# Kernel tuning notes

Measured on AMD Instinct MI355X. Metric: run time of the kernel, lower is better.

Reference implementation:

```python
import jax, jax.numpy as jnp
import numpy as np

B = 4096
L = 15          # self.length
NINP = 256      # emb_size
NHID = 512      # hidden_size
VOCAB = 30005
TOPK = 10
K = 4 * TOPK + 2   # 42 actions
N_SPLIT = 2 * TOPK
N_STEP = 5      # num_edits
PAD = 30003


def _lstm_dir(x, Wih, Whh, b, reverse):
    # x: [T,B,D]; Wih: [4H,D]; Whh: [4H,H]; b: [4H] (b_ih+b_hh). PyTorch gate order i,f,g,o.
    Bsz, H = x.shape[1], Whh.shape[1]
    def step(carry, xt):
        h, c = carry
        z = xt @ Wih.T + h @ Whh.T + b
        i, f, g, o = jnp.split(z, 4, axis=-1)
        c = jax.nn.sigmoid(f) * c + jax.nn.sigmoid(i) * jnp.tanh(g)
        h = jax.nn.sigmoid(o) * jnp.tanh(c)
        return (h, c), h
    h0 = jnp.zeros((Bsz, H), x.dtype)
    _, ys = jax.lax.scan(step, (h0, h0), x, reverse=reverse)
    return ys  # [T,B,H], position-aligned for both directions


def bilstm(x, Wih0, Whh0, b0, Wih1, Whh1, b1):
    # x: [B,T,D] -> [B,T,2H]; 2-layer bidirectional, zero initial state (matches c0/h0 zeros).
    xt = jnp.swapaxes(x, 0, 1)
    for Wih, Whh, b in ((Wih0, Whh0, b0), (Wih1, Whh1, b1)):
        fw = _lstm_dir(xt, Wih[0], Whh[0], b[0], False)
        bw = _lstm_dir(xt, Wih[1], Whh[1], b[1], True)
        xt = jnp.concatenate([fw, bw], axis=-1)
    return jnp.swapaxes(xt, 0, 1)


def policy_step(st_1, length_t, pos, emb0, key_pos, rep_words, valid_id,
                emb_table, enc_table, Wih0, Whh0, b0, Wih1, Whh1, b1,
                del_vec, hold_vec, mlp_W, mlp_b, mlp1_W, mlp1_b):
    Bsz = st_1.shape[0]
    pos_row = jnp.zeros((L,), jnp.float32).at[pos].set(1.0)         # static pos
    pos_tensor = jnp.broadcast_to(pos_row[None, :, None], (Bsz, L, 1))
    embt = emb_table[st_1] * (1.0 - pos_tensor)
    x = jnp.concatenate([embt, emb0, pos_tensor], axis=2)            # [B,L,2*ninp+1]
    out = bilstm(x, Wih0, Whh0, b0, Wih1, Whh1, b1)                  # [B,L,2*nhid]
    pooled = out[:, pos, :]
    representation = jnp.concatenate(
        [pooled, key_pos[:, pos:pos + 1], jnp.broadcast_to(pos_row[None, :], (Bsz, L))], axis=1)
    # external encoder output is detached in the original
    word_emb = jax.lax.stop_gradient(enc_table[rep_words])           # [B,4*topk,ninp]
    emb2 = jnp.concatenate([word_emb,
                            jnp.broadcast_to(del_vec, (Bsz, 1, NINP)),
                            jnp.broadcast_to(hold_vec, (Bsz, 1, NINP))], axis=1)  # [B,K,ninp]
    onehot = jnp.broadcast_to(jnp.eye(K, dtype=jnp.float32)[None], (Bsz, K, K))
    emb2 = jnp.concatenate([emb2, onehot], axis=2)                   # [B,K,ninp+K]
    rep100 = representation @ mlp_W.T + mlp_b                        # [B,100]
    emb100 = emb2 @ mlp1_W.T + mlp1_b                                # [B,K,100]
    score = jnp.einsum('bkd,bd->bk', emb100, rep100)
    policy = jax.nn.softmax(score, axis=1)
    action = jnp.argmax(policy, axis=1, keepdims=True).astype(jnp.int32)  # eval mode
    pi = jnp.take_along_axis(policy, action, axis=1)                 # [B,1]

    rep_b = (action < N_SPLIT).astype(jnp.int32)
    replaceflag = rep_b * valid_id
    ins_b = ((action >= N_SPLIT) & (action < 2 * N_SPLIT)).astype(jnp.int32)
    insertflag = ins_b * valid_id * (length_t + ins_b <= 15).astype(jnp.int32)
    del_b = (action == 2 * N_SPLIT).astype(jnp.int32)
    deleteflag = del_b * valid_id * (length_t - del_b > 2).astype(jnp.int32)
    holdflag = 1 - replaceflag - insertflag - deleteflag

    action_words = jnp.take_along_axis(rep_words, jnp.clip(action, 0, N_SPLIT - 1), axis=1)  # [B,1]
    rep_seq = jnp.concatenate([action_words, st_1[:, pos + 1:]], axis=1)
    ins_seq = jnp.concatenate([action_words, st_1[:, pos:-1]], axis=1)
    padding = jnp.full((Bsz, 1), PAD, dtype=st_1.dtype)
    del_seq = jnp.concatenate([st_1[:, pos + 1:], padding], axis=1)
    hol_seq = st_1[:, pos:]
    new_tail = (rep_seq * replaceflag + ins_seq * insertflag
                + del_seq * deleteflag + hol_seq * holdflag)
    st = st_1.at[:, pos:].set(new_tail)
    length_tt = insertflag + length_t - deleteflag
    return st, pi, action.astype(jnp.float32), length_tt


def setup_inputs() -> dict:
    key = jax.random.key(0)
    ks = jax.random.split(key, 20)
    s = 0.05
    in0 = 2 * NINP + 1
    in1 = 2 * NHID
    inp = {
        'input_ids': jax.random.randint(ks[0], (B, L), 0, 30000, dtype=jnp.int32),
        'key_pos': jax.random.uniform(ks[1], (B, L), dtype=jnp.float32),
        'sequence_length': jax.random.randint(ks[2], (B, 1), 3, 16, dtype=jnp.int32),
        'rep_words_all': jax.random.randint(ks[3], (B, N_STEP, 4 * TOPK), 0, 30000, dtype=jnp.int32),
        'valid_id_all': jax.random.randint(ks[4], (B, N_STEP, 1), 0, 2, dtype=jnp.int32),
        'emb_table': jax.random.normal(ks[5], (VOCAB, NINP), jnp.float32) * s,
        'enc_table': jax.random.normal(ks[6], (VOCAB, NINP), jnp.float32) * s,
        'Wih0': jax.random.normal(ks[7], (2, 4 * NHID, in0), jnp.float32) * s,
        'Whh0': jax.random.normal(ks[8], (2, 4 * NHID, NHID), jnp.float32) * s,
        'b0': jax.random.normal(ks[9], (2, 4 * NHID), jnp.float32) * s,
        'Wih1': jax.random.normal(ks[10], (2, 4 * NHID, in1), jnp.float32) * s,
        'Whh1': jax.random.normal(ks[11], (2, 4 * NHID, NHID), jnp.float32) * s,
        'b1': jax.random.normal(ks[12], (2, 4 * NHID), jnp.float32) * s,
        'del_vec': jax.random.uniform(ks[13], (1, 1, NINP), dtype=jnp.float32),
        'hold_vec': jax.random.uniform(ks[14], (1, 1, NINP), dtype=jnp.float32),
        'mlp_W': jax.random.normal(ks[15], (100, 2 * NHID + 1 + L), jnp.float32) * s,
        'mlp_b': jnp.zeros((100,), jnp.float32),
        'mlp1_W': jax.random.normal(ks[16], (100, NINP + K), jnp.float32) * s,
        'mlp1_b': jnp.zeros((100,), jnp.float32),
    }
    return inp


def reference(input_ids, key_pos, sequence_length, rep_words_all, valid_id_all,
              emb_table, enc_table, Wih0, Whh0, b0, Wih1, Whh1, b1,
              del_vec, hold_vec, mlp_W, mlp_b, mlp1_W, mlp1_b):
    st = input_ids
    emb0 = emb_table[input_ids]            # embedding of s0, computed once
    length_t = sequence_length
    pis, acts = [], []
    for i in range(N_STEP):
        pos = i % (L - 3) + 2              # static per unrolled step
        st, pi, a, length_t = policy_step(
            st, length_t, pos, emb0, key_pos,
            rep_words_all[:, i, :], valid_id_all[:, i, :],
            emb_table, enc_table, Wih0, Whh0, b0, Wih1, Whh1, b1,
            del_vec, hold_vec, mlp_W, mlp_b, mlp1_W, mlp1_b)
        pis.append(pi)
        acts.append(a)
    pis = jnp.concatenate(pis, axis=1)     # [B,N_STEP]
    actions = jnp.concatenate(acts, axis=1)
    return pis, actions, st, length_t
```

## Files before the change

kernel.cpp:

```cpp
#include <hip/hip_runtime.h>

#define B_ 4096
#define L_ 15
#define NSTEP_ 5
#define VOC_ 30005
#define PAD_ 30003

typedef _Float16 f16;
typedef f16  f16x8 __attribute__((ext_vector_type(8)));
typedef float f32x16 __attribute__((ext_vector_type(16)));

__device__ __forceinline__ float sigf(float x){ return 1.0f/(1.0f+expf(-x)); }

#define MFMA_(d,a,b) d = __builtin_amdgcn_mfma_f32_32x32x16_f16(a,b,d,0,0,0)

struct RecParams {
  const f16 *A1h_0,*A1l_0,*A1h_1,*A1l_1;
  const f16 *A2h_0,*A2l_0,*A2h_1,*A2l_1;
  const f16 *Wfh_0,*Wfl_0,*Wfh_1,*Wfl_1;
  const float *bias_0,*bias_1;
  const f16 *embH,*embL;
  const int *st,*ids;
  float *c_0,*c_1,*h2_0,*h2_1;
  f16 *hh_0,*hl_0,*hh_1,*hl_1;
  int lda1, lda2, ldh, ldh2, k1p, k2p, first, gather, t_0, t_1, pos, b0c, act0, act1;
};

__device__ __forceinline__ int swz(int row, int s){
  int u = ((row&7)<<1) | s;
  return ((row>>3)<<8) + ((u ^ (u>>1))<<4);
}

__global__ __launch_bounds__(256,2) void rec_gemm(RecParams p){
  const int dir = blockIdx.z;
  if (!(dir ? p.act1 : p.act0)) return;
  const f16* A1h = dir ? p.A1h_1 : p.A1h_0;
  const f16* A1l = dir ? p.A1l_1 : p.A1l_0;
  const f16* A2h = dir ? p.A2h_1 : p.A2h_0;
  const f16* A2l = dir ? p.A2l_1 : p.A2l_0;
  const f16* Wfh = dir ? p.Wfh_1 : p.Wfh_0;
  const f16* Wfl = dir ? p.Wfl_1 : p.Wfl_0;
  const float* bias = dir ? p.bias_1 : p.bias_0;
  float* cbuf = dir ? p.c_1 : p.c_0;
  float* h2   = dir ? p.h2_1 : p.h2_0;
  f16* hhb = dir ? p.hh_1 : p.hh_0;
  f16* hlb = dir ? p.hl_1 : p.hl_0;
  const int tcur = dir ? p.t_1 : p.t_0;

  const int tid  = threadIdx.x;
  const int lane = tid & 63;
  const int w    = tid >> 6;
  const int mbase = blockIdx.y*128;

  __shared__ union {
    float z[128*128];
    f16   stg[8][2048];
  } sm;

  f32x16 accM[2][2], accX[2][2];
#pragma unroll
  for (int i=0;i<2;i++)
#pragma unroll
    for (int j=0;j<2;j++)
#pragma unroll
      for (int r=0;r<16;r++){ accM[i][j][r]=0.f; accX[i][j][r]=0.f; }

  const int arow = (w&1)*64 + (lane&31);
  const int fs = lane>>5;
  const int aoff0 = swz(arow,    fs), aoff1 = swz(arow+32, fs);

  const int ct0 = blockIdx.x*4 + (w>>1)*2;
  const f16* WfhL = Wfh + (size_t)lane*8;
  const f16* WflL = Wfl + (size_t)lane*8;

  const int srow = tid >> 1, ss = tid & 1;
  const int sws = swz(srow, ss);
  const int ktot = p.k1p + p.k2p;

  int tokT=0, tokI=0, zflag=0;
  if (p.gather){
    int gb = p.b0c + mbase + srow;
    tokT = p.st [gb*L_ + tcur];
    tokI = p.ids[gb*L_ + tcur];
    zflag = (tcur == p.pos) ? 1 : 0;
  }

  f16x8 ra_h0, ra_l0, ra_h1, ra_l1;
  const f16x8 zero8 = {0,0,0,0,0,0,0,0};

  auto gload = [&](int ph){
    if (ph >= ktot) return;
    if (ph < p.k1p){
      if (p.gather){
        if (ph < 8){
          if (zflag){ ra_h0=zero8; ra_l0=zero8; ra_h1=zero8; ra_l1=zero8; }
          else {
            size_t base = (size_t)tokT*256 + ph*32 + ss*8;
            ra_h0 = *(const f16x8*)(p.embH + base);
            ra_l0 = *(const f16x8*)(p.embL + base);
            ra_h1 = *(const f16x8*)(p.embH + base + 16);
            ra_l1 = *(const f16x8*)(p.embL + base + 16);
          }
        } else if (ph < 16){
          size_t base = (size_t)tokI*256 + (ph-8)*32 + ss*8;
          ra_h0 = *(const f16x8*)(p.embH + base);
          ra_l0 = *(const f16x8*)(p.embL + base);
          ra_h1 = *(const f16x8*)(p.embH + base + 16);
          ra_l1 = *(const f16x8*)(p.embL + base + 16);
        } else {
          ra_h0 = zero8; ra_l0 = zero8; ra_h1 = zero8; ra_l1 = zero8;
          if (ss == 0) ra_h0[0] = zflag ? (f16)1.0f : (f16)0.0f;
        }
      } else {
        long base = (long)(mbase+srow)*p.lda1 + ph*32 + ss*8;
        ra_h0 = *(const f16x8*)(A1h + base);
        ra_l0 = *(const f16x8*)(A1l + base);
        ra_h1 = *(const f16x8*)(A1h + base + 16);
        ra_l1 = *(const f16x8*)(A1l + base + 16);
      }
    } else {
      long base = (long)(mbase+srow)*p.lda2 + (ph - p.k1p)*32 + ss*8;
      ra_h0 = *(const f16x8*)(A2h + base);
      ra_l0 = *(const f16x8*)(A2l + base);
      ra_h1 = *(const f16x8*)(A2h + base + 16);
      ra_l1 = *(const f16x8*)(A2l + base + 16);
    }
  };
  auto swrite = [&](int buf){
    *(f16x8*)((char*)sm.stg[buf*4+0] + sws) = ra_h0;
    *(f16x8*)((char*)sm.stg[buf*4+1] + sws) = ra_l0;
    *(f16x8*)((char*)sm.stg[buf*4+2] + sws) = ra_h1;
    *(f16x8*)((char*)sm.stg[buf*4+3] + sws) = ra_l1;
  };

  gload(0); swrite(0); gload(1);
  __syncthreads();

  for (int ph=0; ph<ktot; ++ph){
    const int cur = ph & 1;
    size_t base0 = ((size_t)(ph*2+0)*64 + ct0)*512;
    size_t base1 = ((size_t)(ph*2+1)*64 + ct0)*512;
    f16x8 rbh00 = *(const f16x8*)(WfhL + base0);
    f16x8 rbh01 = *(const f16x8*)(WfhL + base0 + 512);
    f16x8 rbl00 = *(const f16x8*)(WflL + base0);
    f16x8 rbl01 = *(const f16x8*)(WflL + base0 + 512);
    f16x8 rbh10 = *(const f16x8*)(WfhL + base1);
    f16x8 rbh11 = *(const f16x8*)(WfhL + base1 + 512);
    f16x8 rbl10 = *(const f16x8*)(WflL + base1);
    f16x8 rbl11 = *(const f16x8*)(WflL + base1 + 512);
    const char* s0h = (const char*)sm.stg[cur*4+0];
    const char* s0l = (const char*)sm.stg[cur*4+1];
    const char* s1h = (const char*)sm.stg[cur*4+2];
    const char* s1l = (const char*)sm.stg[cur*4+3];
    f16x8 a00h = *(const f16x8*)(s0h + aoff0);
    f16x8 a01h = *(const f16x8*)(s0h + aoff1);
    f16x8 a00l = *(const f16x8*)(s0l + aoff0);
    f16x8 a01l = *(const f16x8*)(s0l + aoff1);
    f16x8 a10h = *(const f16x8*)(s1h + aoff0);
    f16x8 a11h = *(const f16x8*)(s1h + aoff1);
    f16x8 a10l = *(const f16x8*)(s1l + aoff0);
    f16x8 a11l = *(const f16x8*)(s1l + aoff1);
    if (ph+1 < ktot){ swrite((ph+1)&1); gload(ph+2); }
    MFMA_(accM[0][0], a00h, rbh00); MFMA_(accX[0][0], a00h, rbl00); MFMA_(accX[0][0], a00l, rbh00);
    MFMA_(accM[1][0], a01h, rbh00); MFMA_(accX[1][0], a01h, rbl00); MFMA_(accX[1][0], a01l, rbh00);
    MFMA_(accM[0][1], a00h, rbh01); MFMA_(accX[0][1], a00h, rbl01); MFMA_(accX[0][1], a00l, rbh01);
    MFMA_(accM[1][1], a01h, rbh01); MFMA_(accX[1][1], a01h, rbl01); MFMA_(accX[1][1], a01l, rbh01);
    MFMA_(accM[0][0], a10h, rbh10); MFMA_(accX[0][0], a10h, rbl10); MFMA_(accX[0][0], a10l, rbh10);
    MFMA_(accM[1][0], a11h, rbh10); MFMA_(accX[1][0], a11h, rbl10); MFMA_(accX[1][0], a11l, rbh10);
    MFMA_(accM[0][1], a10h, rbh11); MFMA_(accX[0][1], a10h, rbl11); MFMA_(accX[0][1], a10l, rbh11);
    MFMA_(accM[1][1], a11h, rbh11); MFMA_(accX[1][1], a11h, rbl11); MFMA_(accX[1][1], a11l, rbh11);
    __syncthreads();
  }

#pragma unroll
  for (int tm=0;tm<2;tm++)
#pragma unroll
   for (int tn=0;tn<2;tn++){
    int lcol = (w>>1)*64 + tn*32 + (lane&31);
    float bv = bias[blockIdx.x*128 + lcol];
#pragma unroll
    for (int r=0;r<16;r++){
      int lrow = (w&1)*64 + tm*32 + (r&3) + 8*(r>>2) + 4*(lane>>5);
      sm.z[lrow*128 + lcol] = accM[tm][tn][r] + 0.000244140625f*accX[tm][tn][r] + bv;
    }
   }
  __syncthreads();

  const int nb = blockIdx.x*32;
#pragma unroll
  for (int it=0; it<16; ++it){
    int idx = it*256 + tid;
    int nq = idx & 31, row = idx >> 5;
    float4 g4 = *(const float4*)&sm.z[row*128 + nq*4];
    int m = mbase + row, n = nb + nq;
    float cp = p.first ? 0.f : cbuf[(size_t)m*512 + n];
    float cc = sigf(g4.y)*cp + sigf(g4.x)*tanhf(g4.z);
    float hv = sigf(g4.w)*tanhf(cc);
    cbuf[(size_t)m*512 + n] = cc;
    f16 hi = (f16)hv;
    f16 lo = (f16)((hv - (float)hi)*4096.0f);
    hhb[(size_t)m*p.ldh + n] = hi;
    hlb[(size_t)m*p.ldh + n] = lo;
    if (h2) h2[(size_t)m*p.ldh2 + n] = hv;
  }
}

__global__ void prep_w0(const float* Wih, const float* Whh, const float* b0,
                        f16* Wfh, f16* Wfl, float* bp){
  int gid = blockIdx.x*blockDim.x + threadIdx.x;
  const int PER_DIR = 66*64*64*8;
  if (gid >= 2*PER_DIR) return;
  int dir = gid / PER_DIR;
  int rem = gid % PER_DIR;
  int j = rem & 7, lane = (rem>>3)&63, ct = (rem>>9)&63, kt16 = rem>>15;
  int n4g = ct*32 + (lane&31);
  int n = n4g>>2, g = n4g&3;
  int srow = dir*2048 + g*512 + n;
  int k = kt16*16 + ((lane>>5)<<3) + j;
  float v;
  if (k < 513)       v = Wih[(size_t)srow*513 + k];
  else if (k < 544)  v = 0.f;
  else               v = Whh[(size_t)srow*512 + (k-544)];
  f16 hi = (f16)v;
  Wfh[gid] = hi;
  Wfl[gid] = (f16)((v - (float)hi)*4096.0f);
  if (kt16==0 && (lane>>5)==0 && j==0) bp[dir*2048 + n4g] = b0[srow];
}

__global__ void prep_w1(const float* Wih, const float* Whh, const float* b1,
                        f16* Wfh, f16* Wfl, float* bp){
  int gid = blockIdx.x*blockDim.x + threadIdx.x;
  const int PER_DIR = 96*64*64*8;
  if (gid >= 2*PER_DIR) return;
  int dir = gid / PER_DIR;
  int rem = gid % PER_DIR;
  int j = rem & 7, lane = (rem>>3)&63, ct = (rem>>9)&63, kt16 = rem>>15;
  int n4g = ct*32 + (lane&31);
  int n = n4g>>2, g = n4g&3;
  int srow = dir*2048 + g*512 + n;
  int k = kt16*16 + ((lane>>5)<<3) + j;
  float v;
  if (k < 1024) v = Wih[(size_t)srow*1024 + k];
  else          v = Whh[(size_t)srow*512 + (k-1024)];
  f16 hi = (f16)v;
  Wfh[gid] = hi;
  Wfl[gid] = (f16)((v - (float)hi)*4096.0f);
  if (kt16==0 && (lane>>5)==0 && j==0) bp[dir*2048 + n4g] = b1[srow];
}

__global__ void prep_emb(const float* emb, f16* eh, f16* el){
  int gid = blockIdx.x*blockDim.x + threadIdx.x;
  if (gid >= VOC_*256) return;
  float v = emb[gid];
  f16 hi = (f16)v;
  eh[gid] = hi;
  el[gid] = (f16)((v - (float)hi)*4096.0f);
}

__global__ void prep_mlpwt(const float* mW, float* wt){
  int gid = blockIdx.x*blockDim.x + threadIdx.x;
  if (gid >= 100*1040) return;
  int j = gid / 1040, k = gid % 1040;
  wt[k*100 + j] = mW[gid];
}

__global__ __launch_bounds__(128) void prep_encproj(const float* enc, const float* delv,
                        const float* holdv, const float* m1W, const float* m1b, float* ep){
  int r = blockIdx.x;
  __shared__ float row[256];
  const float* src = (r < VOC_) ? enc + (size_t)r*256 : (r == VOC_ ? delv : holdv);
  for (int i=threadIdx.x;i<256;i+=128) row[i]=src[i];
  __syncthreads();
  int j = threadIdx.x;
  if (j < 100){
    double s = (double)m1b[j];
    const float* wr = m1W + (size_t)j*298;
    for (int k=0;k<256;k++) s += (double)wr[k] * (double)row[k];
    ep[(size_t)r*100 + j] = (float)s;
  }
}

__global__ void init_st(const int* ids, const int* seqlen, int* st, int* len){
  int gid = blockIdx.x*blockDim.x + threadIdx.x;
  if (gid < B_*L_) st[gid] = ids[gid];
  if (gid < B_)    len[gid] = seqlen[gid];
}

__global__ void sentinel(float* out, float v){
  int gid = blockIdx.x*blockDim.x + threadIdx.x;
  if (gid < B_*NSTEP_) out[gid] = v;
}

__global__ __launch_bounds__(128) void score_update(
    const float* pooled, const float* keypos, const float* mWt, const float* mb,
    const float* ep, const float* m1W, const int* repw, const int* valid,
    int* st, int* len, float* outPis, float* outActs, int step, int pos, int b0){
  int b = blockIdx.x;
  int bg = b0 + b;
  __shared__ float rep[1040];
  __shared__ float r100[100];
  __shared__ double sc[42];
  int tid = threadIdx.x;
  for (int i=tid;i<1024;i+=128) rep[i] = pooled[(size_t)b*1024+i];
  if (tid < 16){
    if (tid == 0) rep[1024] = keypos[bg*L_+pos];
    else          rep[1024+tid] = ((tid-1)==pos) ? 1.f : 0.f;
  }
  __syncthreads();
  if (tid < 100){
    double s = (double)mb[tid];
    for (int k=0;k<1040;k++) s += (double)mWt[k*100+tid] * (double)rep[k];
    r100[tid] = (float)s;
  }
  __syncthreads();
  if (tid < 42){
    int row = (tid < 40) ? repw[((size_t)bg*NSTEP_+step)*40 + tid] : (VOC_ + (tid-40));
    const float* er = ep + (size_t)row*100;
    double s = 0.0;
    for (int j=0;j<100;j++) s += (double)er[j] * (double)r100[j];
    for (int j=0;j<100;j++) s += (double)m1W[j*298 + 256 + tid] * (double)r100[j];
    sc[tid] = s;
  }
  __syncthreads();
  if (tid == 0){
    double mx = sc[0]; int am = 0;
    for (int k=1;k<42;k++) if (sc[k] > mx){ mx = sc[k]; am = k; }
    double sum = 0.0;
    for (int k=0;k<42;k++) sum += exp(sc[k]-mx);
    float pi = (float)(1.0/sum);
    int vid = valid[bg*NSTEP_+step];
    int ln  = len[bg];
    int repb = (am < 20) ? 1 : 0;
    int insb = (am >= 20 && am < 40) ? 1 : 0;
    int delb = (am == 40) ? 1 : 0;
    int repf = repb*vid;
    int insf = insb*vid*(((ln+insb) <= 15) ? 1 : 0);
    int delf = delb*vid*(((ln-delb) >  2) ? 1 : 0);
    int T = L_ - pos;
    int tail[13];
    for (int j=0;j<T;j++) tail[j] = st[bg*L_+pos+j];
    int aw = repw[((size_t)bg*NSTEP_+step)*40 + (am < 20 ? am : 19)];
    for (int j=0;j<T;j++){
      int rv = (j==0) ? aw : tail[j];
      int iv = (j==0) ? aw : tail[j-1];
      int dv = (j < T-1) ? tail[j+1] : PAD_;
      int hv = tail[j];
      int nv = repf ? rv : (insf ? iv : (delf ? dv : hv));
      st[bg*L_+pos+j] = nv;
    }
    len[bg] = ln + insf - delf;
    outPis[bg*NSTEP_+step]  = pi;
    outActs[bg*NSTEP_+step] = (float)am;
  }
}

__global__ void finalize(const int* st, const int* len, float* out){
  int gid = blockIdx.x*blockDim.x + threadIdx.x;
  if (gid < B_*L_)            out[2*B_*NSTEP_ + gid] = (float)st[gid];
  else if (gid < B_*L_ + B_)  out[2*B_*NSTEP_ + B_*L_ + (gid - B_*L_)] = (float)len[gid - B_*L_];
}

extern "C" void kernel_launch(void* const* d_in, const int* in_sizes, int n_in,
                              void* d_out, int out_size, void* d_ws, size_t ws_size,
                              hipStream_t stream) {
  const int*   ids    = (const int*)  d_in[0];
  const float* keypos = (const float*)d_in[1];
  const int*   seqlen = (const int*)  d_in[2];
  const int*   repw   = (const int*)  d_in[3];
  const int*   valid  = (const int*)  d_in[4];
  const float* emb    = (const float*)d_in[5];
  const float* enc    = (const float*)d_in[6];
  const float* Wih0   = (const float*)d_in[7];
  const float* Whh0   = (const float*)d_in[8];
  const float* b0     = (const float*)d_in[9];
  const float* Wih1   = (const float*)d_in[10];
  const float* Whh1   = (const float*)d_in[11];
  const float* b1     = (const float*)d_in[12];
  const float* delv   = (const float*)d_in[13];
  const float* holdv  = (const float*)d_in[14];
  const float* mW     = (const float*)d_in[15];
  const float* mb     = (const float*)d_in[16];
  const float* m1W    = (const float*)d_in[17];
  const float* m1b    = (const float*)d_in[18];
  float* out = (float*)d_out;

  const int NKW0 = 66, NKW1 = 96;
  const size_t W0PD = (size_t)NKW0*64*64*8;
  const size_t W1PD = (size_t)NKW1*64*64*8;

  char* ws = (char*)d_ws;
  size_t off = 0;
  auto allocB = [&](size_t bytes) -> char* {
    char* pp = ws + off; off += (bytes + 255) & ~size_t(255); return pp;
  };
  f16*  Wf0h = (f16*)allocB(2*W0PD*2);
  f16*  Wf0l = (f16*)allocB(2*W0PD*2);
  f16*  Wf1h = (f16*)allocB(2*W1PD*2);
  f16*  Wf1l = (f16*)allocB(2*W1PD*2);
  float* bp0 = (float*)allocB(4096*4);
  float* bp1 = (float*)allocB(4096*4);
  f16*  embH = (f16*)allocB((size_t)VOC_*256*2);
  f16*  embL = (f16*)allocB((size_t)VOC_*256*2);
  float* mWt = (float*)allocB(104000*4);
  float* ep  = (float*)allocB((size_t)30007*100*4);
  int* stbuf  = (int*)allocB(B_*L_*4);
  int* lenbuf = (int*)allocB(B_*4);
  size_t fixedB = off;

  const int cands[6] = {4096, 2048, 1024, 512, 256, 128};
  int Bc = 0;
  for (int ci=0; ci<6; ++ci){
    size_t c = cands[ci];
    size_t chunkB = c*(size_t)(15*1024*2*2 + 4*512*2*2 + 2*512*4 + 2*512*4 + 1024*4) + 8*256;
    if (fixedB + chunkB <= ws_size){ Bc = (int)c; break; }
  }
  if (!Bc){
    float code = 100000.0f + (float)(ws_size >> 20);
    sentinel<<<(B_*NSTEP_+255)/256,256,0,stream>>>(out, code);
    return;
  }
  f16* o0h = (f16*)allocB((size_t)L_*Bc*1024*2);
  f16* o0l = (f16*)allocB((size_t)L_*Bc*1024*2);
  f16* h1h = (f16*)allocB((size_t)4*Bc*512*2);
  f16* h1l = (f16*)allocB((size_t)4*Bc*512*2);
  float* c0 = (float*)allocB((size_t)2*Bc*512*4);
  float* c1 = (float*)allocB((size_t)2*Bc*512*4);
  float* pooled = (float*)allocB((size_t)Bc*1024*4);

  prep_w0<<<(int)((2*W0PD+255)/256),256,0,stream>>>(Wih0, Whh0, b0, Wf0h, Wf0l, bp0);
  prep_w1<<<(int)((2*W1PD+255)/256),256,0,stream>>>(Wih1, Whh1, b1, Wf1h, Wf1l, bp1);
  prep_emb<<<(VOC_*256+255)/256,256,0,stream>>>(emb, embH, embL);
  prep_mlpwt<<<(100*1040+255)/256,256,0,stream>>>(mW, mWt);
  prep_encproj<<<30007,128,0,stream>>>(enc, delv, holdv, m1W, m1b, ep);
  init_st<<<(B_*L_+255)/256,256,0,stream>>>(ids, seqlen, stbuf, lenbuf);

  for (int b0c=0; b0c<B_; b0c+=Bc){
    for (int step=0; step<NSTEP_; ++step){
      int pos = step + 2;

      for (int ts=0; ts<L_; ++ts){
        int tf = ts, tb = 14-ts;
        RecParams p{};
        p.gather = 1; p.t_0 = tf; p.t_1 = tb; p.pos = pos; p.b0c = b0c;
        p.embH = embH; p.embL = embL; p.st = stbuf; p.ids = ids;
        p.k1p = 17; p.k2p = ts ? 16 : 0;
        size_t of0 = (size_t)(ts?tf-1:0)*Bc*1024;
        size_t of1 = (size_t)(ts?tb+1:0)*Bc*1024 + (ts?512:0);
        p.A2h_0 = o0h + of0;  p.A2l_0 = o0l + of0;
        p.A2h_1 = o0h + of1;  p.A2l_1 = o0l + of1;
        p.lda2 = 1024;
        p.Wfh_0 = Wf0h;        p.Wfl_0 = Wf0l;
        p.Wfh_1 = Wf0h + W0PD; p.Wfl_1 = Wf0l + W0PD;
        p.bias_0 = bp0; p.bias_1 = bp0 + 2048;
        p.c_0 = c0; p.c_1 = c0 + (size_t)Bc*512;
        p.hh_0 = o0h + (size_t)tf*Bc*1024;       p.hl_0 = o0l + (size_t)tf*Bc*1024;
        p.hh_1 = o0h + (size_t)tb*Bc*1024 + 512; p.hl_1 = o0l + (size_t)tb*Bc*1024 + 512;
        p.ldh = 1024;
        p.h2_0 = nullptr; p.h2_1 = nullptr; p.ldh2 = 1024;
        p.first = (ts==0); p.act0 = 1; p.act1 = 1;
        rec_gemm<<<dim3(16,Bc/128,2),256,0,stream>>>(p);
      }

      int nL1 = L_ - pos;
      for (int ts=0; ts<nL1; ++ts){
        RecParams p{};
        int tf = ts, tb = 14-ts;
        int parR = (ts-1)&1, parW = ts&1;
        p.gather = 0;
        p.A1h_0 = o0h + (size_t)tf*Bc*1024;  p.A1l_0 = o0l + (size_t)tf*Bc*1024;
        p.A1h_1 = o0h + (size_t)tb*Bc*1024;  p.A1l_1 = o0l + (size_t)tb*Bc*1024;
        p.lda1 = 1024; p.k1p = 32;
        p.k2p  = ts ? 16 : 0;
        size_t r0 = (size_t)(0*2 + (ts?parR:0))*Bc*512;
        size_t r1 = (size_t)(1*2 + (ts?parR:0))*Bc*512;
        p.A2h_0 = h1h + r0; p.A2l_0 = h1l + r0;
        p.A2h_1 = h1h + r1; p.A2l_1 = h1l + r1;
        p.lda2 = 512;
        p.Wfh_0 = Wf1h;        p.Wfl_0 = Wf1l;
        p.Wfh_1 = Wf1h + W1PD; p.Wfl_1 = Wf1l + W1PD;
        p.bias_0 = bp1; p.bias_1 = bp1 + 2048;
        p.c_0 = c1; p.c_1 = c1 + (size_t)Bc*512;
        size_t w0 = (size_t)(0*2 + parW)*Bc*512;
        size_t w1 = (size_t)(1*2 + parW)*Bc*512;
        p.hh_0 = h1h + w0; p.hl_0 = h1l + w0;
        p.hh_1 = h1h + w1; p.hl_1 = h1l + w1;
        p.ldh = 512;
        p.h2_0 = (ts == pos)    ? pooled        : nullptr;
        p.h2_1 = (ts == 14-pos) ? (pooled+512)  : nullptr;
        p.ldh2 = 1024;
        p.first = (ts==0);
        p.act0 = (ts <= pos) ? 1 : 0; p.act1 = 1;
        rec_gemm<<<dim3(16,Bc/128,2),256,0,stream>>>(p);
      }

      score_update<<<Bc,128,0,stream>>>(pooled, keypos, mWt, mb, ep, m1W, repw, valid,
                                        stbuf, lenbuf, out, out + B_*NSTEP_, step, pos, b0c);
    }
  }
  finalize<<<(B_*L_+B_+255)/256,256,0,stream>>>(stbuf, lenbuf, out);
}
```

Measured before the change: 18.52 ms.

## Prefetch B weight fragments one phase ahead and fold direction into grid x

Weight fragments for the next K phase are now loaded into registers after the current MFMAs are issued, so global-load latency overlaps with compute instead of stalling each phase. The full __syncthreads is replaced by an LDS-only waitcnt plus a raw s_barrier, so outstanding global loads no longer have to drain at each barrier. The direction index moves from blockIdx.z into blockIdx.x, which changes block scheduling order so both directions interleave across tiles. The prefetch keeps eight more vector registers live, which may hurt occupancy under the two-blocks-per-SM launch bound.

```diff
diff --git a/kernel.cpp b/kernel.cpp
--- a/kernel.cpp
+++ b/kernel.cpp
@@ -32,7 +32,9 @@
 }
 
 __global__ __launch_bounds__(256,2) void rec_gemm(RecParams p){
-  const int dir = blockIdx.z;
+  const int bxe = blockIdx.x;
+  const int ct4 = bxe & 15;
+  const int dir = bxe >> 4;
   if (!(dir ? p.act1 : p.act0)) return;
   const f16* A1h = dir ? p.A1h_1 : p.A1h_0;
   const f16* A1l = dir ? p.A1l_1 : p.A1l_0;
@@ -69,7 +71,7 @@
   const int fs = lane>>5;
   const int aoff0 = swz(arow,    fs), aoff1 = swz(arow+32, fs);
 
-  const int ct0 = blockIdx.x*4 + (w>>1)*2;
+  const int ct0 = ct4*4 + (w>>1)*2;
   const f16* WfhL = Wfh + (size_t)lane*8;
   const f16* WflL = Wfl + (size_t)lane*8;
 
@@ -132,22 +134,27 @@
     *(f16x8*)((char*)sm.stg[buf*4+2] + sws) = ra_h1;
     *(f16x8*)((char*)sm.stg[buf*4+3] + sws) = ra_l1;
   };
+  auto loadB = [&](int ph, f16x8* rb){
+    size_t base0 = ((size_t)(ph*2+0)*64 + ct0)*512;
+    size_t base1 = ((size_t)(ph*2+1)*64 + ct0)*512;
+    rb[0] = *(const f16x8*)(WfhL + base0);
+    rb[1] = *(const f16x8*)(WfhL + base0 + 512);
+    rb[2] = *(const f16x8*)(WflL + base0);
+    rb[3] = *(const f16x8*)(WflL + base0 + 512);
+    rb[4] = *(const f16x8*)(WfhL + base1);
+    rb[5] = *(const f16x8*)(WfhL + base1 + 512);
+    rb[6] = *(const f16x8*)(WflL + base1);
+    rb[7] = *(const f16x8*)(WflL + base1 + 512);
+  };
 
   gload(0); swrite(0); gload(1);
-  __syncthreads();
+  f16x8 rb[8];
+  loadB(0, rb);
+  asm volatile("s_waitcnt lgkmcnt(0)" ::: "memory");
+  __builtin_amdgcn_s_barrier();
 
   for (int ph=0; ph<ktot; ++ph){
     const int cur = ph & 1;
-    size_t base0 = ((size_t)(ph*2+0)*64 + ct0)*512;
-    size_t base1 = ((size_t)(ph*2+1)*64 + ct0)*512;
-    f16x8 rbh00 = *(const f16x8*)(WfhL + base0);
-    f16x8 rbh01 = *(const f16x8*)(WfhL + base0 + 512);
-    f16x8 rbl00 = *(const f16x8*)(WflL + base0);
-    f16x8 rbl01 = *(const f16x8*)(WflL + base0 + 512);
-    f16x8 rbh10 = *(const f16x8*)(WfhL + base1);
-    f16x8 rbh11 = *(const f16x8*)(WfhL + base1 + 512);
-    f16x8 rbl10 = *(const f16x8*)(WflL + base1);
-    f16x8 rbl11 = *(const f16x8*)(WflL + base1 + 512);
     const char* s0h = (const char*)sm.stg[cur*4+0];
     const char* s0l = (const char*)sm.stg[cur*4+1];
     const char* s1h = (const char*)sm.stg[cur*4+2];
@@ -161,15 +168,17 @@
     f16x8 a10l = *(const f16x8*)(s1l + aoff0);
     f16x8 a11l = *(const f16x8*)(s1l + aoff1);
     if (ph+1 < ktot){ swrite((ph+1)&1); gload(ph+2); }
-    MFMA_(accM[0][0], a00h, rbh00); MFMA_(accX[0][0], a00h, rbl00); MFMA_(accX[0][0], a00l, rbh00);
-    MFMA_(accM[1][0], a01h, rbh00); MFMA_(accX[1][0], a01h, rbl00); MFMA_(accX[1][0], a01l, rbh00);
-    MFMA_(accM[0][1], a00h, rbh01); MFMA_(accX[0][1], a00h, rbl01); MFMA_(accX[0][1], a00l, rbh01);
-    MFMA_(accM[1][1], a01h, rbh01); MFMA_(accX[1][1], a01h, rbl01); MFMA_(accX[1][1], a01l, rbh01);
-    MFMA_(accM[0][0], a10h, rbh10); MFMA_(accX[0][0], a10h, rbl10); MFMA_(accX[0][0], a10l, rbh10);
-    MFMA_(accM[1][0], a11h, rbh10); MFMA_(accX[1][0], a11h, rbl10); MFMA_(accX[1][0], a11l, rbh10);
-    MFMA_(accM[0][1], a10h, rbh11); MFMA_(accX[0][1], a10h, rbl11); MFMA_(accX[0][1], a10l, rbh11);
-    MFMA_(accM[1][1], a11h, rbh11); MFMA_(accX[1][1], a11h, rbl11); MFMA_(accX[1][1], a11l, rbh11);
-    __syncthreads();
+    MFMA_(accM[0][0], a00h, rb[0]); MFMA_(accX[0][0], a00h, rb[2]); MFMA_(accX[0][0], a00l, rb[0]);
+    MFMA_(accM[1][0], a01h, rb[0]); MFMA_(accX[1][0], a01h, rb[2]); MFMA_(accX[1][0], a01l, rb[0]);
+    MFMA_(accM[0][1], a00h, rb[1]); MFMA_(accX[0][1], a00h, rb[3]); MFMA_(accX[0][1], a00l, rb[1]);
+    MFMA_(accM[1][1], a01h, rb[1]); MFMA_(accX[1][1], a01h, rb[3]); MFMA_(accX[1][1], a01l, rb[1]);
+    MFMA_(accM[0][0], a10h, rb[4]); MFMA_(accX[0][0], a10h, rb[6]); MFMA_(accX[0][0], a10l, rb[4]);
+    MFMA_(accM[1][0], a11h, rb[4]); MFMA_(accX[1][0], a11h, rb[6]); MFMA_(accX[1][0], a11l, rb[4]);
+    MFMA_(accM[0][1], a10h, rb[5]); MFMA_(accX[0][1], a10h, rb[7]); MFMA_(accX[0][1], a10l, rb[5]);
+    MFMA_(accM[1][1], a11h, rb[5]); MFMA_(accX[1][1], a11h, rb[7]); MFMA_(accX[1][1], a11l, rb[5]);
+    if (ph+1 < ktot) loadB(ph+1, rb);
+    asm volatile("s_waitcnt lgkmcnt(0)" ::: "memory");
+    __builtin_amdgcn_s_barrier();
   }
 
 #pragma unroll
@@ -177,7 +186,7 @@
 #pragma unroll
    for (int tn=0;tn<2;tn++){
     int lcol = (w>>1)*64 + tn*32 + (lane&31);
-    float bv = bias[blockIdx.x*128 + lcol];
+    float bv = bias[ct4*128 + lcol];
 #pragma unroll
     for (int r=0;r<16;r++){
       int lrow = (w&1)*64 + tm*32 + (r&3) + 8*(r>>2) + 4*(lane>>5);
@@ -186,7 +195,7 @@
    }
   __syncthreads();
 
-  const int nb = blockIdx.x*32;
+  const int nb = ct4*32;
 #pragma unroll
   for (int it=0; it<16; ++it){
     int idx = it*256 + tid;
@@ -458,7 +467,7 @@
         p.ldh = 1024;
         p.h2_0 = nullptr; p.h2_1 = nullptr; p.ldh2 = 1024;
         p.first = (ts==0); p.act0 = 1; p.act1 = 1;
-        rec_gemm<<<dim3(16,Bc/128,2),256,0,stream>>>(p);
+        rec_gemm<<<dim3(32,Bc/128),256,0,stream>>>(p);
       }
 
       int nL1 = L_ - pos;
@@ -490,7 +499,7 @@
         p.ldh2 = 1024;
         p.first = (ts==0);
         p.act0 = (ts <= pos) ? 1 : 0; p.act1 = 1;
-        rec_gemm<<<dim3(16,Bc/128,2),256,0,stream>>>(p);
+        rec_gemm<<<dim3(32,Bc/128),256,0,stream>>>(p);
       }
 
       score_update<<<Bc,128,0,stream>>>(pooled, keypos, mWt, mb, ep, m1W, repw, valid,
```

New measurement: 21.43 ms. +15.8%, slower.
